# Performance work log

Hardware: AMD Instinct MI355X
Metric: run time of the kernel (lower is better)

The kernel has to match this reference:

```python
import jax, jax.numpy as jnp
import numpy as np

N_NODES = 100000
N_EDGES = 400000
D_FEAT = 128
HIDDEN = 64
BETA = 1.0  # temperature default in concrete_sample


def setup_inputs() -> dict:
    key = jax.random.key(0)
    k = jax.random.split(key, 6)
    embed = jax.random.normal(k[0], (N_NODES, D_FEAT), dtype=jnp.float32)
    # elayers: Linear(4*F, 64) -> ReLU -> Linear(64, 1)
    W1 = jax.random.normal(k[1], (4 * D_FEAT, HIDDEN), dtype=jnp.float32) * (1.0 / np.sqrt(4 * D_FEAT))
    b1 = jnp.zeros((HIDDEN,), dtype=jnp.float32)
    W2 = jax.random.normal(k[2], (HIDDEN, 1), dtype=jnp.float32) * (1.0 / np.sqrt(HIDDEN))
    b2 = jnp.zeros((1,), dtype=jnp.float32)
    # per-edge uniform noise, as in torch.rand(w.size()); keep away from {0,1}
    noise = jax.random.uniform(k[3], (N_EDGES,), dtype=jnp.float32, minval=1e-6, maxval=1.0 - 1e-6)
    col = jax.random.randint(k[4], (N_EDGES,), 0, N_NODES, dtype=jnp.int64 if jax.config.jax_enable_x64 else jnp.int32)
    row = jax.random.randint(k[5], (N_EDGES,), 0, N_NODES, dtype=jnp.int64 if jax.config.jax_enable_x64 else jnp.int32)
    return {"embed": embed, "W1": W1, "b1": b1, "W2": W2, "b2": b2,
            "noise": noise, "col": col, "row": row, "src_idx": 0, "dst_idx": 1}


def reference(embed, W1, b1, W2, b2, noise, col, row, src_idx, dst_idx):
    E = col.shape[0]
    F = embed.shape[1]
    # gather per-edge endpoint embeddings + broadcast explained src/dst embeddings
    col_emb = embed[col]                                    # [E, F]
    row_emb = embed[row]                                    # [E, F]
    src_emb = jnp.broadcast_to(embed[src_idx], (E, F))       # [E, F]
    dst_emb = jnp.broadcast_to(embed[dst_idx], (E, F))       # [E, F]
    emb = jnp.concatenate([col_emb, row_emb, src_emb, dst_emb], axis=-1)  # [E, 4F]
    # elayers MLP
    h = jax.nn.relu(emb @ W1 + b1)                          # [E, 64]
    w = (h @ W2 + b2).reshape(-1)                           # [E]
    # concrete_sample (training=True, sample_bias=0): logit(noise) + w, sigmoid
    gate_inputs = (jnp.log(noise) - jnp.log1p(-noise) + w) / BETA
    values = jax.nn.sigmoid(gate_inputs)                    # [E] edge mask
    return values
```

## Files before the change

kernel.cpp:

```cpp
#include <hip/hip_runtime.h>
#include <hip/hip_bf16.h>


typedef __bf16 bf16x8 __attribute__((ext_vector_type(8)));
typedef float  f32x16 __attribute__((ext_vector_type(16)));
typedef unsigned short u16;

#define W1T_LDS_STRIDE 264
#define Z16 {0.f,0.f,0.f,0.f,0.f,0.f,0.f,0.f,0.f,0.f,0.f,0.f,0.f,0.f,0.f,0.f}

__device__ __forceinline__ unsigned bfbits(float f){
  unsigned u = __builtin_bit_cast(unsigned, f);
  return (u + 0x7fffu + ((u >> 16) & 1u)) >> 16;
}
__device__ __forceinline__ unsigned pk2(float a, float b){
  return bfbits(a) | (bfbits(b) << 16);
}
__device__ __forceinline__ float bflo(unsigned u){ return __builtin_bit_cast(float, u << 16); }
__device__ __forceinline__ float bfhi(unsigned u){ return __builtin_bit_cast(float, u & 0xffff0000u); }

__global__ void prep_kernel(const float* __restrict__ embed, const float* __restrict__ W1,
                            const float* __restrict__ b1, const int* __restrict__ srcp,
                            const int* __restrict__ dstp, float* __restrict__ c_ws,
                            u16* __restrict__ w1t)
{
  int b = blockIdx.x, tid = threadIdx.x;
  if (b == 64){
    if (tid < 64){
      int si = srcp[0], di = dstp[0];
      const float* se = embed + (size_t)si * 128;
      const float* de = embed + (size_t)di * 128;
      float acc = b1[tid];
      #pragma unroll 4
      for (int k = 0; k < 128; ++k){
        acc += se[k] * W1[(256 + k) * 64 + tid];
        acc += de[k] * W1[(384 + k) * 64 + tid];
      }
      c_ws[tid] = acc;
    }
    return;
  }
  int n = tid & 63;
  int k = b * 4 + (tid >> 6);
  w1t[n * 256 + k] = (u16)bfbits(W1[k * 64 + n]);
}

__global__ __launch_bounds__(256, 3) void fg_kernel(
    const float* __restrict__ embed, const u16* __restrict__ w1t,
    const float* __restrict__ c_ws, u16* __restrict__ F, u16* __restrict__ G, int NN)
{
  __shared__ __align__(16) u16 sW[64 * W1T_LDS_STRIDE];
  __shared__ float sC[64];
  int tid = threadIdx.x;
  for (int i = tid; i < 2048; i += 256){
    uint4 v = ((const uint4*)w1t)[i];
    int e0 = i * 8, n = e0 >> 8, kk = e0 & 255;
    *(uint4*)&sW[n * W1T_LDS_STRIDE + kk] = v;
  }
  if (tid < 64) sC[tid] = c_ws[tid];
  __syncthreads();
  int lane = tid & 63, wave = tid >> 6;
  int nl = lane & 31, h5 = lane >> 5;
  int tile = blockIdx.x * 128 + wave * 32;
  if (tile >= NN) return;
  const float* erow = embed + (size_t)(tile + nl) * 128;
  f32x16 aF0 = Z16, aF1 = Z16, aG0 = Z16, aG1 = Z16;
  const u16* sw0 = sW + nl * W1T_LDS_STRIDE;
  const u16* sw1 = sW + (32 + nl) * W1T_LDS_STRIDE;
  #pragma unroll
  for (int s = 0; s < 8; ++s){
    int ko = s * 16 + h5 * 8;
    float4 x = *(const float4*)(erow + ko);
    float4 y = *(const float4*)(erow + ko + 4);
    uint4 u; u.x = pk2(x.x,x.y); u.y = pk2(x.z,x.w); u.z = pk2(y.x,y.y); u.w = pk2(y.z,y.w);
    bf16x8 a = __builtin_bit_cast(bf16x8, u);
    bf16x8 bF0 = *(const bf16x8*)(sw0 + ko);
    bf16x8 bF1 = *(const bf16x8*)(sw1 + ko);
    bf16x8 bG0 = *(const bf16x8*)(sw0 + 128 + ko);
    bf16x8 bG1 = *(const bf16x8*)(sw1 + 128 + ko);
    aF0 = __builtin_amdgcn_mfma_f32_32x32x16_bf16(a, bF0, aF0, 0, 0, 0);
    aF1 = __builtin_amdgcn_mfma_f32_32x32x16_bf16(a, bF1, aF1, 0, 0, 0);
    aG0 = __builtin_amdgcn_mfma_f32_32x32x16_bf16(a, bG0, aG0, 0, 0, 0);
    aG1 = __builtin_amdgcn_mfma_f32_32x32x16_bf16(a, bG1, aG1, 0, 0, 0);
  }
  float cv0 = sC[nl], cv1 = sC[32 + nl];
  #pragma unroll
  for (int r = 0; r < 16; ++r){
    int node = tile + (r & 3) + 8 * (r >> 2) + 4 * h5;
    u16* fr = F + (size_t)node * 64 + nl;
    u16* gr = G + (size_t)node * 64 + nl;
    fr[0]  = (u16)bfbits(aF0[r] + cv0);
    fr[32] = (u16)bfbits(aF1[r] + cv1);
    gr[0]  = (u16)bfbits(aG0[r]);
    gr[32] = (u16)bfbits(aG1[r]);
  }
}

__global__ __launch_bounds__(256, 8) void edge_kernel(
    const u16* __restrict__ F, const u16* __restrict__ G,
    const float* __restrict__ W2, const float* __restrict__ b2,
    const float* __restrict__ noise, const int* __restrict__ col,
    const int* __restrict__ row, float* __restrict__ out, int E)
{
  int tid = threadIdx.x;
  int lane = tid & 63, wave = tid >> 6;
  int j = lane & 7, grp = lane >> 3;
  float4 w2a = ((const float4*)W2)[2 * j];
  float4 w2b = ((const float4*)W2)[2 * j + 1];
  float b2v = b2[0];
  int base = blockIdx.x * 256 + wave * 64;
  #pragma unroll 2
  for (int it = 0; it < 8; ++it){
    int e0 = base + it * 8;
    if (e0 >= E) break;
    int e = e0 + grp;
    int ci = col[e], ri = row[e];
    uint4 fv = ((const uint4*)(F + (size_t)ci * 64))[j];
    uint4 gv = ((const uint4*)(G + (size_t)ri * 64))[j];
    float p = 0.f, h;
    h = fmaxf(bflo(fv.x) + bflo(gv.x), 0.f); p += h * w2a.x;
    h = fmaxf(bfhi(fv.x) + bfhi(gv.x), 0.f); p += h * w2a.y;
    h = fmaxf(bflo(fv.y) + bflo(gv.y), 0.f); p += h * w2a.z;
    h = fmaxf(bfhi(fv.y) + bfhi(gv.y), 0.f); p += h * w2a.w;
    h = fmaxf(bflo(fv.z) + bflo(gv.z), 0.f); p += h * w2b.x;
    h = fmaxf(bfhi(fv.z) + bfhi(gv.z), 0.f); p += h * w2b.y;
    h = fmaxf(bflo(fv.w) + bflo(gv.w), 0.f); p += h * w2b.z;
    h = fmaxf(bfhi(fv.w) + bfhi(gv.w), 0.f); p += h * w2b.w;
    p += __shfl_xor(p, 1, 64);
    p += __shfl_xor(p, 2, 64);
    p += __shfl_xor(p, 4, 64);
    if (j == 0){
      float ns = noise[e];
      float g = logf(ns) - log1pf(-ns) + p + b2v;
      out[e] = 1.f / (1.f + expf(-g));
    }
  }
}

__global__ void naive_kernel(const float* __restrict__ embed, const float* __restrict__ W1,
    const float* __restrict__ b1, const float* __restrict__ W2, const float* __restrict__ b2,
    const float* __restrict__ noise, const int* __restrict__ col, const int* __restrict__ row,
    const int* __restrict__ srcp, const int* __restrict__ dstp, float* __restrict__ out, int E)
{
  int e = blockIdx.x * 256 + threadIdx.x;
  if (e >= E) return;
  int ci = col[e], ri = row[e], si = srcp[0], di = dstp[0];
  const float* ce = embed + (size_t)ci * 128;
  const float* re = embed + (size_t)ri * 128;
  const float* se = embed + (size_t)si * 128;
  const float* de = embed + (size_t)di * 128;
  float w = b2[0];
  for (int jj = 0; jj < 64; ++jj){
    float hh = b1[jj];
    for (int k = 0; k < 128; ++k){
      hh += ce[k] * W1[k * 64 + jj] + re[k] * W1[(128 + k) * 64 + jj]
          + se[k] * W1[(256 + k) * 64 + jj] + de[k] * W1[(384 + k) * 64 + jj];
    }
    w += fmaxf(hh, 0.f) * W2[jj];
  }
  float ns = noise[e];
  float g = logf(ns) - log1pf(-ns) + w;
  out[e] = 1.f / (1.f + expf(-g));
}

extern "C" void kernel_launch(void* const* d_in, const int* in_sizes, int n_in,
                              void* d_out, int out_size, void* d_ws, size_t ws_size,
                              hipStream_t stream)
{
  const float* embed = (const float*)d_in[0];
  const float* W1    = (const float*)d_in[1];
  const float* b1    = (const float*)d_in[2];
  const float* W2    = (const float*)d_in[3];
  const float* b2    = (const float*)d_in[4];
  const float* noise = (const float*)d_in[5];
  const int*   col   = (const int*)d_in[6];
  const int*   rowp  = (const int*)d_in[7];
  const int*   srcp  = (const int*)d_in[8];
  const int*   dstp  = (const int*)d_in[9];
  const int E  = in_sizes[5];
  const int NN = in_sizes[0] / 128;
  float* out = (float*)d_out;

  const size_t fOff   = 33280;
  const size_t fBytes = (size_t)NN * 64 * sizeof(u16);
  const size_t need   = fOff + 2 * fBytes;

  if (ws_size >= need){
    float* c_ws = (float*)d_ws;
    u16*   w1t  = (u16*)((char*)d_ws + 256);
    u16*   F    = (u16*)((char*)d_ws + fOff);
    u16*   G    = (u16*)((char*)d_ws + fOff + fBytes);
    prep_kernel<<<65, 256, 0, stream>>>(embed, W1, b1, srcp, dstp, c_ws, w1t);
    fg_kernel<<<(NN + 127) / 128, 256, 0, stream>>>(embed, w1t, c_ws, F, G, NN);
    edge_kernel<<<(E + 255) / 256, 256, 0, stream>>>(F, G, W2, b2, noise, col, rowp, out, E);
  } else {
    naive_kernel<<<(E + 255) / 256, 256, 0, stream>>>(embed, W1, b1, W2, b2, noise,
                                                      col, rowp, srcp, dstp, out, E);
  }
}
```

Measured before the change: 142.8 us.

## Fold prep into fg_kernel and make edge_kernel one edge-group per wave

Removes the separate prep kernel: each fg_kernel block now converts and transposes W1 into LDS itself and computes the constant src/dst bias contribution with a 4-way split reduction. This drops one kernel launch and its workspace round trip, at the cost of every block redundantly reading W1 (128 KB) and the src/dst rows. The edge kernel also changes from each wave looping over 64 edges to each wave handling 8 edges with no loop, launching many more blocks to raise parallelism for the gather.

```diff
diff --git a/kernel.cpp b/kernel.cpp
--- a/kernel.cpp
+++ b/kernel.cpp
@@ -6,7 +6,7 @@
 typedef float  f32x16 __attribute__((ext_vector_type(16)));
 typedef unsigned short u16;
 
-#define W1T_LDS_STRIDE 264
+#define WSTR 264
 #define Z16 {0.f,0.f,0.f,0.f,0.f,0.f,0.f,0.f,0.f,0.f,0.f,0.f,0.f,0.f,0.f,0.f}
 
 __device__ __forceinline__ unsigned bfbits(float f){
@@ -19,54 +19,53 @@
 __device__ __forceinline__ float bflo(unsigned u){ return __builtin_bit_cast(float, u << 16); }
 __device__ __forceinline__ float bfhi(unsigned u){ return __builtin_bit_cast(float, u & 0xffff0000u); }
 
-__global__ void prep_kernel(const float* __restrict__ embed, const float* __restrict__ W1,
-                            const float* __restrict__ b1, const int* __restrict__ srcp,
-                            const int* __restrict__ dstp, float* __restrict__ c_ws,
-                            u16* __restrict__ w1t)
+__global__ __launch_bounds__(256, 3) void fg_kernel(
+    const float* __restrict__ embed, const float* __restrict__ W1,
+    const float* __restrict__ b1, const int* __restrict__ srcp,
+    const int* __restrict__ dstp, u16* __restrict__ F, u16* __restrict__ G, int NN)
 {
-  int b = blockIdx.x, tid = threadIdx.x;
-  if (b == 64){
-    if (tid < 64){
-      int si = srcp[0], di = dstp[0];
-      const float* se = embed + (size_t)si * 128;
-      const float* de = embed + (size_t)di * 128;
-      float acc = b1[tid];
-      #pragma unroll 4
-      for (int k = 0; k < 128; ++k){
-        acc += se[k] * W1[(256 + k) * 64 + tid];
-        acc += de[k] * W1[(384 + k) * 64 + tid];
-      }
-      c_ws[tid] = acc;
+  __shared__ __align__(16) u16 sW[64 * WSTR];
+  __shared__ float sC[64];
+  __shared__ float sRed[256];
+  int tid = threadIdx.x;
+
+  #pragma unroll
+  for (int i = 0; i < 16; ++i){
+    int idx = i * 256 + tid;
+    int k = idx >> 4, q = idx & 15;
+    float4 v = *(const float4*)(W1 + k * 64 + q * 4);
+    sW[(4*q+0) * WSTR + k] = (u16)bfbits(v.x);
+    sW[(4*q+1) * WSTR + k] = (u16)bfbits(v.y);
+    sW[(4*q+2) * WSTR + k] = (u16)bfbits(v.z);
+    sW[(4*q+3) * WSTR + k] = (u16)bfbits(v.w);
+  }
+  {
+    int h = tid & 63, part = tid >> 6;
+    int si = srcp[0], di = dstp[0];
+    const float* se  = embed + (size_t)si * 128 + part * 32;
+    const float* de  = embed + (size_t)di * 128 + part * 32;
+    const float* w1s = W1 + (256 + part * 32) * 64 + h;
+    const float* w1d = W1 + (384 + part * 32) * 64 + h;
+    float acc = 0.f;
+    #pragma unroll 8
+    for (int k = 0; k < 32; ++k){
+      acc += se[k] * w1s[k * 64];
+      acc += de[k] * w1d[k * 64];
     }
-    return;
+    sRed[tid] = acc;
   }
-  int n = tid & 63;
-  int k = b * 4 + (tid >> 6);
-  w1t[n * 256 + k] = (u16)bfbits(W1[k * 64 + n]);
-}
+  __syncthreads();
+  if (tid < 64) sC[tid] = b1[tid] + sRed[tid] + sRed[64+tid] + sRed[128+tid] + sRed[192+tid];
+  __syncthreads();
 
-__global__ __launch_bounds__(256, 3) void fg_kernel(
-    const float* __restrict__ embed, const u16* __restrict__ w1t,
-    const float* __restrict__ c_ws, u16* __restrict__ F, u16* __restrict__ G, int NN)
-{
-  __shared__ __align__(16) u16 sW[64 * W1T_LDS_STRIDE];
-  __shared__ float sC[64];
-  int tid = threadIdx.x;
-  for (int i = tid; i < 2048; i += 256){
-    uint4 v = ((const uint4*)w1t)[i];
-    int e0 = i * 8, n = e0 >> 8, kk = e0 & 255;
-    *(uint4*)&sW[n * W1T_LDS_STRIDE + kk] = v;
-  }
-  if (tid < 64) sC[tid] = c_ws[tid];
-  __syncthreads();
   int lane = tid & 63, wave = tid >> 6;
   int nl = lane & 31, h5 = lane >> 5;
   int tile = blockIdx.x * 128 + wave * 32;
   if (tile >= NN) return;
   const float* erow = embed + (size_t)(tile + nl) * 128;
   f32x16 aF0 = Z16, aF1 = Z16, aG0 = Z16, aG1 = Z16;
-  const u16* sw0 = sW + nl * W1T_LDS_STRIDE;
-  const u16* sw1 = sW + (32 + nl) * W1T_LDS_STRIDE;
+  const u16* sw0 = sW + nl * WSTR;
+  const u16* sw1 = sW + (32 + nl) * WSTR;
   #pragma unroll
   for (int s = 0; s < 8; ++s){
     int ko = s * 16 + h5 * 8;
@@ -105,35 +104,30 @@
   int tid = threadIdx.x;
   int lane = tid & 63, wave = tid >> 6;
   int j = lane & 7, grp = lane >> 3;
+  int e0 = blockIdx.x * 32 + wave * 8;
+  if (e0 >= E) return;
+  int e = e0 + grp; if (e >= E) e = E - 1;
+  int ci = col[e], ri = row[e];
+  uint4 fv = ((const uint4*)(F + (size_t)ci * 64))[j];
+  uint4 gv = ((const uint4*)(G + (size_t)ri * 64))[j];
   float4 w2a = ((const float4*)W2)[2 * j];
   float4 w2b = ((const float4*)W2)[2 * j + 1];
-  float b2v = b2[0];
-  int base = blockIdx.x * 256 + wave * 64;
-  #pragma unroll 2
-  for (int it = 0; it < 8; ++it){
-    int e0 = base + it * 8;
-    if (e0 >= E) break;
-    int e = e0 + grp;
-    int ci = col[e], ri = row[e];
-    uint4 fv = ((const uint4*)(F + (size_t)ci * 64))[j];
-    uint4 gv = ((const uint4*)(G + (size_t)ri * 64))[j];
-    float p = 0.f, h;
-    h = fmaxf(bflo(fv.x) + bflo(gv.x), 0.f); p += h * w2a.x;
-    h = fmaxf(bfhi(fv.x) + bfhi(gv.x), 0.f); p += h * w2a.y;
-    h = fmaxf(bflo(fv.y) + bflo(gv.y), 0.f); p += h * w2a.z;
-    h = fmaxf(bfhi(fv.y) + bfhi(gv.y), 0.f); p += h * w2a.w;
-    h = fmaxf(bflo(fv.z) + bflo(gv.z), 0.f); p += h * w2b.x;
-    h = fmaxf(bfhi(fv.z) + bfhi(gv.z), 0.f); p += h * w2b.y;
-    h = fmaxf(bflo(fv.w) + bflo(gv.w), 0.f); p += h * w2b.z;
-    h = fmaxf(bfhi(fv.w) + bfhi(gv.w), 0.f); p += h * w2b.w;
-    p += __shfl_xor(p, 1, 64);
-    p += __shfl_xor(p, 2, 64);
-    p += __shfl_xor(p, 4, 64);
-    if (j == 0){
-      float ns = noise[e];
-      float g = logf(ns) - log1pf(-ns) + p + b2v;
-      out[e] = 1.f / (1.f + expf(-g));
-    }
+  float p = 0.f, h;
+  h = fmaxf(bflo(fv.x) + bflo(gv.x), 0.f); p += h * w2a.x;
+  h = fmaxf(bfhi(fv.x) + bfhi(gv.x), 0.f); p += h * w2a.y;
+  h = fmaxf(bflo(fv.y) + bflo(gv.y), 0.f); p += h * w2a.z;
+  h = fmaxf(bfhi(fv.y) + bfhi(gv.y), 0.f); p += h * w2a.w;
+  h = fmaxf(bflo(fv.z) + bflo(gv.z), 0.f); p += h * w2b.x;
+  h = fmaxf(bfhi(fv.z) + bfhi(gv.z), 0.f); p += h * w2b.y;
+  h = fmaxf(bflo(fv.w) + bflo(gv.w), 0.f); p += h * w2b.z;
+  h = fmaxf(bfhi(fv.w) + bfhi(gv.w), 0.f); p += h * w2b.w;
+  p += __shfl_xor(p, 1, 64);
+  p += __shfl_xor(p, 2, 64);
+  p += __shfl_xor(p, 4, 64);
+  if (j == 0 && e0 + grp < E){
+    float ns = noise[e];
+    float g = logf(ns) - log1pf(-ns) + p + b2[0];
+    out[e] = 1.f / (1.f + expf(-g));
   }
 }
 
@@ -181,18 +175,12 @@
   const int NN = in_sizes[0] / 128;
   float* out = (float*)d_out;
 
-  const size_t fOff   = 33280;
   const size_t fBytes = (size_t)NN * 64 * sizeof(u16);
-  const size_t need   = fOff + 2 * fBytes;
-
-  if (ws_size >= need){
-    float* c_ws = (float*)d_ws;
-    u16*   w1t  = (u16*)((char*)d_ws + 256);
-    u16*   F    = (u16*)((char*)d_ws + fOff);
-    u16*   G    = (u16*)((char*)d_ws + fOff + fBytes);
-    prep_kernel<<<65, 256, 0, stream>>>(embed, W1, b1, srcp, dstp, c_ws, w1t);
-    fg_kernel<<<(NN + 127) / 128, 256, 0, stream>>>(embed, w1t, c_ws, F, G, NN);
-    edge_kernel<<<(E + 255) / 256, 256, 0, stream>>>(F, G, W2, b2, noise, col, rowp, out, E);
+  if (ws_size >= 2 * fBytes){
+    u16* F = (u16*)d_ws;
+    u16* G = (u16*)((char*)d_ws + fBytes);
+    fg_kernel<<<(NN + 127) / 128, 256, 0, stream>>>(embed, W1, b1, srcp, dstp, F, G, NN);
+    edge_kernel<<<(E + 31) / 32, 256, 0, stream>>>(F, G, W2, b2, noise, col, rowp, out, E);
   } else {
     naive_kernel<<<(E + 255) / 256, 256, 0, stream>>>(embed, W1, b1, W2, b2, noise,
                                                       col, rowp, srcp, dstp, out, E);
```

After: 134.0 us (median of 3 runs). 6.2% less time.
